# Kernel optimization log

Hardware: AMD Instinct MI355X
Metric: run time of the kernel (lower is better)

The kernel has to match this reference:

```python
import jax, jax.numpy as jnp
import numpy as np

WIDTH = 768
HEAD = 64

def setup_inputs() -> dict:
    key = jax.random.key(0)
    ks = jax.random.split(key, 8)
    x = jax.random.normal(ks[0], (8, 2048, WIDTH), dtype=jnp.float32)
    mask = jax.random.randint(ks[1], (2048, 2048), 0, 2, dtype=jnp.int32)
    s = 1.0 / np.sqrt(WIDTH)
    Wq = jax.random.normal(ks[2], (WIDTH, HEAD), dtype=jnp.float32) * s
    Wk = jax.random.normal(ks[3], (WIDTH, HEAD), dtype=jnp.float32) * s
    Wv = jax.random.normal(ks[4], (WIDTH, HEAD), dtype=jnp.float32) * s
    bq = jax.random.normal(ks[5], (HEAD,), dtype=jnp.float32) * 0.01
    bk = jax.random.normal(ks[6], (HEAD,), dtype=jnp.float32) * 0.01
    bv = jax.random.normal(ks[7], (HEAD,), dtype=jnp.float32) * 0.01
    return {"x": x, "Wq": Wq, "bq": bq, "Wk": Wk, "bk": bk, "Wv": Wv, "bv": bv, "mask": mask}

def reference(x, Wq, bq, Wk, bk, Wv, bv, mask) -> jnp.ndarray:
    # x: [B, N, width]; projections -> [B, N, head]
    Q = jnp.einsum('bnw,wh->bnh', x, Wq) + bq
    K = jnp.einsum('bnw,wh->bnh', x, Wk) + bk
    V = jnp.einsum('bnw,wh->bnh', x, Wv) + bv
    scale = 1.0 / jnp.sqrt(jnp.asarray(Q.shape[-1], dtype=Q.dtype))
    scores = jnp.einsum('bqh,bkh->bqk', Q, K) * scale  # [B, N, N]
    scores = jnp.where(mask == 0, -jnp.inf, scores)
    attn = jax.nn.softmax(scores, axis=-1)
    return jnp.einsum('bqk,bkh->bqh', attn, V)
```

## Files before the change

### kernel.cpp

```cpp
#include <hip/hip_runtime.h>

typedef short  s8v   __attribute__((ext_vector_type(8)));
typedef float  f32x4 __attribute__((ext_vector_type(4)));

#define SEQ 2048
#define WID 768

__device__ __forceinline__ unsigned fbits(float f) {
    union { float f; unsigned u; } v; v.f = f; return v.u;
}
__device__ __forceinline__ float bitsf(unsigned u) {
    union { unsigned u; float f; } v; v.u = u; return v.f;
}
__device__ __forceinline__ unsigned short f2b(float f) {
    unsigned u = fbits(f);
    return (unsigned short)((u + 0x7FFFu + ((u >> 16) & 1u)) >> 16);
}
__device__ __forceinline__ unsigned packRNE(float a, float b) {
    unsigned ta = fbits(a) + 0x7FFFu + ((fbits(a) >> 16) & 1u);
    unsigned tb = fbits(b) + 0x7FFFu + ((fbits(b) >> 16) & 1u);
    return __builtin_amdgcn_perm(tb, ta, 0x07060302u);
}
__device__ __forceinline__ unsigned packTRUNC(float a, float b) {
    return __builtin_amdgcn_perm(fbits(b), fbits(a), 0x07060302u);
}
__device__ __forceinline__ f32x4 zero4() { f32x4 z = {0.f, 0.f, 0.f, 0.f}; return z; }

__device__ __forceinline__ void async16(const unsigned short* g, unsigned short* l) {
    __builtin_amdgcn_global_load_lds(
        (const __attribute__((address_space(1))) unsigned int*)g,
        (__attribute__((address_space(3))) unsigned int*)l, 16, 0, 0);
}

__global__ __launch_bounds__(256) void convert_kernel(
    const float* __restrict__ x, const int* __restrict__ mask,
    const float* __restrict__ Wq, const float* __restrict__ Wk, const float* __restrict__ Wv,
    unsigned short* __restrict__ XF, unsigned short* __restrict__ WF,
    unsigned* __restrict__ PM)
{
    const int tid = threadIdx.x;
    const int blk = blockIdx.x;
    if (blk < 6144) {
        const unsigned s = blk * 256 + tid;
        const unsigned g = s / 1536;
        const unsigned r = s - g * 1536;
        const unsigned kc32 = r >> 6, l = r & 63;
        const unsigned row = g * 16 + (l & 15);
        const unsigned k0 = kc32 * 32 + (l >> 4) * 8;
        float4 f0 = *(const float4*)&x[(size_t)row * WID + k0];
        float4 f1 = *(const float4*)&x[(size_t)row * WID + k0 + 4];
        uint4 w;
        w.x = packRNE(f0.x, f0.y); w.y = packRNE(f0.z, f0.w);
        w.z = packRNE(f1.x, f1.y); w.w = packRNE(f1.z, f1.w);
        *(uint4*)&XF[(size_t)s * 8] = w;
    } else if (blk < 6656) {
        const int b2 = blk - 6144;
        const int gid  = b2 * 4 + (tid >> 6);
        const int lane = tid & 63, quad = lane >> 4, c = lane & 15;
        const int qb = gid >> 5, kb = gid & 31;
        unsigned w = 0;
        #pragma unroll
        for (int mt = 0; mt < 2; ++mt)
            #pragma unroll
            for (int i = 0; i < 4; ++i) {
                const int q = qb * 32 + mt * 16 + quad * 4 + i;
                const int4 mm = *(const int4*)&mask[(size_t)q * SEQ + kb * 64 + 4 * c];
                if (mm.x) w |= 1u << (mt * 16 + i * 4 + 0);
                if (mm.y) w |= 1u << (mt * 16 + i * 4 + 1);
                if (mm.z) w |= 1u << (mt * 16 + i * 4 + 2);
                if (mm.w) w |= 1u << (mt * 16 + i * 4 + 3);
            }
        PM[(size_t)gid * 64 + lane] = w;
    } else {
        const int s2 = (blk - 6656) * 256 + tid;
        const int chunk = s2 >> 6, l = s2 & 63;
        const int ntg = chunk / 24, r = chunk - ntg * 24;
        const int kc = r >> 1, h = r & 1;
        const int mat = ntg >> 2;
        const int col = (ntg & 3) * 16 + (l & 15);
        const int k0 = kc * 64 + h * 32 + (l >> 4) * 8;
        const float* Wm = (mat == 0) ? Wq : (mat == 1) ? Wk : Wv;
        float p[8];
        #pragma unroll
        for (int j = 0; j < 8; ++j) p[j] = Wm[(size_t)(k0 + j) * 64 + col];
        uint4 w;
        w.x = packRNE(p[0], p[1]); w.y = packRNE(p[2], p[3]);
        w.z = packRNE(p[4], p[5]); w.w = packRNE(p[6], p[7]);
        *(uint4*)&WF[(size_t)s2 * 8] = w;
    }
}

__global__ __launch_bounds__(512, 4) void qkv_proj_kernel(
    const unsigned short* __restrict__ XF, const unsigned short* __restrict__ WF,
    const float* __restrict__ bq, const float* __restrict__ bk, const float* __restrict__ bv,
    unsigned short* __restrict__ QF, unsigned short* __restrict__ KF,
    unsigned short* __restrict__ VF)
{
    __shared__ unsigned short AB[2][16384];
    unsigned short (*St)[200] = (unsigned short(*)[200])AB;

    const int tid = threadIdx.x;
    const int wv = tid >> 6, lane = tid & 63, quad = lane >> 4, c = lane & 15;
    const int rg = wv >> 2, cg = wv & 3;
    const int blk = blockIdx.x;
    const int g0 = blk * 4;

    float bias[3];
    #pragma unroll
    for (int nt = 0; nt < 3; ++nt) {
        int col = cg * 48 + nt * 16 + c;
        const float* B = (col < 64) ? bq : (col < 128) ? bk : bv;
        bias[nt] = B[col & 63];
    }

    auto issue = [&](int kc, int b) {
        #pragma unroll
        for (int r = 0; r < 4; ++r) {
            const int d = wv * 4 + r;
            if (d < 8) {
                const int gl = d >> 1, h = d & 1;
                async16(XF + ((size_t)(g0 + gl) * 24 + 2 * kc + h) * 512 + lane * 8,
                        &AB[b][(gl * 2 + h) * 512]);
            } else {
                const int e = d - 8, ntg = e >> 1, h = e & 1;
                async16(WF + (((size_t)ntg * 12 + kc) * 2 + h) * 512 + lane * 8,
                        &AB[b][4096 + (ntg * 2 + h) * 512]);
            }
        }
    };

    f32x4 acc[2][3];
    #pragma unroll
    for (int mt = 0; mt < 2; ++mt)
        #pragma unroll
        for (int nt = 0; nt < 3; ++nt) acc[mt][nt] = zero4();

    issue(0, 0);
    for (int kc = 0; kc < 12; ++kc) {
        const int b = kc & 1;
        __syncthreads();
        if (kc < 11) issue(kc + 1, b ^ 1);

        s8v afr[2][2], bfr[3][2];
        #pragma unroll
        for (int mt = 0; mt < 2; ++mt)
            #pragma unroll
            for (int h = 0; h < 2; ++h)
                afr[mt][h] = *(const s8v*)&AB[b][((rg * 2 + mt) * 2 + h) * 512 + lane * 8];
        #pragma unroll
        for (int nt = 0; nt < 3; ++nt)
            #pragma unroll
            for (int h = 0; h < 2; ++h)
                bfr[nt][h] = *(const s8v*)&AB[b][4096 + ((cg * 3 + nt) * 2 + h) * 512 + lane * 8];
        #pragma unroll
        for (int h = 0; h < 2; ++h)
            #pragma unroll
            for (int mt = 0; mt < 2; ++mt)
                #pragma unroll
                for (int nt = 0; nt < 3; ++nt)
                    acc[mt][nt] = __builtin_amdgcn_mfma_f32_16x16x32_bf16(
                        afr[mt][h], bfr[nt][h], acc[mt][nt], 0, 0, 0);
        __syncthreads();
    }

    #pragma unroll
    for (int mt = 0; mt < 2; ++mt)
        #pragma unroll
        for (int nt = 0; nt < 3; ++nt)
            #pragma unroll
            for (int i = 0; i < 4; ++i)
                St[rg * 32 + mt * 16 + quad * 4 + i][cg * 48 + nt * 16 + c]
                    = f2b(acc[mt][nt][i] + bias[nt]);
    __syncthreads();

    {
        const int g = tid >> 7, ks = (tid >> 6) & 1, l = tid & 63;
        uint4 v = *(uint4*)&St[g * 16 + (l & 15)][ks * 32 + (l >> 4) * 8];
        *(uint4*)&QF[(((size_t)(g0 + g)) * 2 + ks) * 512 + (size_t)l * 8] = v;
    }
    {
        const int ksnt = tid >> 6, l = tid & 63;
        const int ks = ksnt >> 2, nt = ksnt & 3;
        uint4 v = *(uint4*)&St[4 * (l & 15) + nt][64 + ks * 32 + (l >> 4) * 8];
        *(uint4*)&KF[(((size_t)blk * 8 + ksnt) * 64 + l) * 8] = v;
    }
    {
        const int ksnt = tid >> 6, l = tid & 63;
        const int ks = ksnt >> 2, nt = ksnt & 3;
        const int d = 128 + nt * 16 + (l & 15);
        const int r0 = ks * 32 + (l >> 4) * 8;
        unsigned short p[8];
        #pragma unroll
        for (int s = 0; s < 8; ++s) p[s] = St[r0 + s][d];
        uint4 w;
        w.x = (unsigned)p[0] | ((unsigned)p[1] << 16);
        w.y = (unsigned)p[2] | ((unsigned)p[3] << 16);
        w.z = (unsigned)p[4] | ((unsigned)p[5] << 16);
        w.w = (unsigned)p[6] | ((unsigned)p[7] << 16);
        *(uint4*)&VF[(((size_t)blk * 8 + ksnt) * 64 + l) * 8] = w;
    }
}

__global__ __launch_bounds__(1024, 4) void attn_kernel(
    const unsigned short* __restrict__ QF, const unsigned short* __restrict__ KF,
    const unsigned short* __restrict__ VF, const unsigned* __restrict__ PM,
    float* __restrict__ out)
{
    __shared__ unsigned short KV[4][8192];
    __shared__ __align__(16) unsigned char PsOb[36864];
    __shared__ float Lbuf[64];
    unsigned short (*Ps)[16][72] = (unsigned short(*)[16][72])PsOb;
    float (*Obuf)[68]            = (float(*)[68])PsOb;

    const int tid = threadIdx.x;
    const int wv = tid >> 6, lane = tid & 63, quad = lane >> 4, c = lane & 15;
    const int sl = wv & 3, qg = wv >> 2, mt = qg & 1;
    const int blk = blockIdx.x;
    const int bb = blk & 7, qt = blk >> 3;
    const size_t qrow0 = (size_t)bb * SEQ + qt * 64;

    if (tid < 64) Lbuf[tid] = 0.f;

    s8v qf[2];
    {
        const size_t qgrp = (size_t)bb * 128 + qt * 4 + qg;
        #pragma unroll
        for (int ks = 0; ks < 2; ++ks)
            qf[ks] = *(const s8v*)&QF[(qgrp * 2 + ks) * 512 + (size_t)lane * 8];
    }

    f32x4 O[4];
    float lro[4];
    #pragma unroll
    for (int nt = 0; nt < 4; ++nt) O[nt] = zero4();
    #pragma unroll
    for (int i = 0; i < 4; ++i) lro[i] = 0.f;

    auto kv_dma = [&](int kt) {
        const size_t kbg = (size_t)bb * 32 + sl * 8 + kt;
        #pragma unroll
        for (int r = 0; r < 4; ++r) {
            const int d = qg * 4 + r;
            const unsigned short* src = (d < 8)
                ? KF + kbg * 4096 + (d & 7) * 512 + lane * 8
                : VF + kbg * 4096 + (d & 7) * 512 + lane * 8;
            async16(src, &KV[sl][(d >> 3) * 4096 + (d & 7) * 512]);
        }
    };

    kv_dma(0);
    for (int kt = 0; kt < 8; ++kt) {
        const unsigned pm = PM[(size_t)((qt * 2 + (qg >> 1)) * 32 + sl * 8 + kt) * 64 + lane];
        __syncthreads();

        f32x4 S[4];
        #pragma unroll
        for (int nt = 0; nt < 4; ++nt) S[nt] = zero4();
        #pragma unroll
        for (int ks = 0; ks < 2; ++ks) {
            s8v kfr[4];
            #pragma unroll
            for (int nt = 0; nt < 4; ++nt)
                kfr[nt] = *(const s8v*)&KV[sl][((ks * 4 + nt) * 64 + lane) * 8];
            #pragma unroll
            for (int nt = 0; nt < 4; ++nt)
                S[nt] = __builtin_amdgcn_mfma_f32_16x16x32_bf16(qf[ks], kfr[nt], S[nt], 0, 0, 0);
        }

        const unsigned pmh = pm >> (mt * 16);
        #pragma unroll
        for (int i = 0; i < 4; ++i) {
            float p4[4];
            #pragma unroll
            for (int nt = 0; nt < 4; ++nt) {
                float e = exp2f(fmaf(S[nt][i], 0.18033688011112042f, -21.640425613334451f));
                p4[nt] = ((pmh >> (i * 4 + nt)) & 1u) ? e : 0.f;
            }
            unsigned u0 = packTRUNC(p4[0], p4[1]);
            unsigned u1 = packTRUNC(p4[2], p4[3]);
            lro[i] += bitsf(u0 << 16) + bitsf(u0 & 0xFFFF0000u)
                    + bitsf(u1 << 16) + bitsf(u1 & 0xFFFF0000u);
            *(uint2*)&Ps[wv][quad * 4 + i][4 * c] = make_uint2(u0, u1);
        }

        #pragma unroll
        for (int ks = 0; ks < 2; ++ks) {
            s8v a = *(const s8v*)&Ps[wv][c][ks * 32 + quad * 8];
            s8v vfr[4];
            #pragma unroll
            for (int nt = 0; nt < 4; ++nt)
                vfr[nt] = *(const s8v*)&KV[sl][4096 + ((ks * 4 + nt) * 64 + lane) * 8];
            #pragma unroll
            for (int nt = 0; nt < 4; ++nt)
                O[nt] = __builtin_amdgcn_mfma_f32_16x16x32_bf16(a, vfr[nt], O[nt], 0, 0, 0);
        }
        __syncthreads();
        if (kt < 7) kv_dma(kt + 1);
    }

    #pragma unroll
    for (int j = 0; j < 5; ++j) {
        int idx = tid + 1024 * j;
        if (idx < 64 * 68) ((float*)Obuf)[idx] = 0.f;
    }
    __syncthreads();
    #pragma unroll
    for (int i = 0; i < 4; ++i) {
        float l = lro[i];
        l += __shfl_xor(l, 1);
        l += __shfl_xor(l, 2);
        l += __shfl_xor(l, 4);
        l += __shfl_xor(l, 8);
        if (c == 0) atomicAdd(&Lbuf[qg * 16 + quad * 4 + i], l);
        #pragma unroll
        for (int nt = 0; nt < 4; ++nt)
            atomicAdd(&Obuf[qg * 16 + quad * 4 + i][nt * 16 + c], O[nt][i]);
    }
    __syncthreads();
    {
        const int r = tid >> 4, d4 = (tid & 15) * 4;
        const float invL = 1.0f / Lbuf[r];
        float4 v = *(float4*)&Obuf[r][d4];
        float4 o = make_float4(v.x * invL, v.y * invL, v.z * invL, v.w * invL);
        *(float4*)&out[(qrow0 + r) * 64 + d4] = o;
    }
}

extern "C" void kernel_launch(void* const* d_in, const int* in_sizes, int n_in,
                              void* d_out, int out_size, void* d_ws, size_t ws_size,
                              hipStream_t stream)
{
    const float* x    = (const float*)d_in[0];
    const float* Wq   = (const float*)d_in[1];
    const float* bq   = (const float*)d_in[2];
    const float* Wk   = (const float*)d_in[3];
    const float* bk   = (const float*)d_in[4];
    const float* Wv   = (const float*)d_in[5];
    const float* bv   = (const float*)d_in[6];
    const int*   mask = (const int*)d_in[7];
    float* out = (float*)d_out;

    unsigned short* QF = (unsigned short*)d_ws;
    unsigned short* KF = QF + (size_t)16384 * 64;
    unsigned short* VF = KF + (size_t)16384 * 64;
    unsigned short* XF = VF + (size_t)16384 * 64;
    unsigned short* WF = XF + (size_t)16384 * WID;
    unsigned*       PM = (unsigned*)(WF + (size_t)192 * WID);

    convert_kernel<<<6728, 256, 0, stream>>>(x, mask, Wq, Wk, Wv, XF, WF, PM);
    qkv_proj_kernel<<<256, 512, 0, stream>>>(XF, WF, bq, bk, bv, QF, KF, VF);
    attn_kernel<<<256, 1024, 0, stream>>>(QF, KF, VF, PM, out);
}
```

Before: 163.5 us.

## Keep P in registers via transposed QK MFMA and double-buffer K/V tiles

The QK^T MFMA now runs with K as the A operand, so each lane's score fragment already matches the layout the PV MFMA needs for P. This removes the LDS round-trip for the probability tile, and the mask bit-packing and V layout are permuted to match. K/V tiles are double-buffered, with two DMAs issued ahead and explicit vmcnt waits plus raw s_barriers replacing __syncthreads. Mask words and Q are preloaded into registers before the loop. The cost is more LDS for the second K/V buffer, fragile hand-tuned waitcnt logic, and higher register pressure.

```diff
diff --git a/kernel.cpp b/kernel.cpp
--- a/kernel.cpp
+++ b/kernel.cpp
@@ -60,16 +60,17 @@
         const int qb = gid >> 5, kb = gid & 31;
         unsigned w = 0;
         #pragma unroll
-        for (int mt = 0; mt < 2; ++mt)
+        for (int mt = 0; mt < 2; ++mt) {
+            const int q = qb * 32 + mt * 16 + c;
             #pragma unroll
             for (int i = 0; i < 4; ++i) {
-                const int q = qb * 32 + mt * 16 + quad * 4 + i;
-                const int4 mm = *(const int4*)&mask[(size_t)q * SEQ + kb * 64 + 4 * c];
+                const int4 mm = *(const int4*)&mask[(size_t)q * SEQ + kb * 64 + quad * 16 + 4 * i];
                 if (mm.x) w |= 1u << (mt * 16 + i * 4 + 0);
                 if (mm.y) w |= 1u << (mt * 16 + i * 4 + 1);
                 if (mm.z) w |= 1u << (mt * 16 + i * 4 + 2);
                 if (mm.w) w |= 1u << (mt * 16 + i * 4 + 3);
             }
+        }
         PM[(size_t)gid * 64 + lane] = w;
     } else {
         const int s2 = (blk - 6656) * 256 + tid;
@@ -188,7 +189,7 @@
         const int ksnt = tid >> 6, l = tid & 63;
         const int ks = ksnt >> 2, nt = ksnt & 3;
         const int d = 128 + nt * 16 + (l & 15);
-        const int r0 = ks * 32 + (l >> 4) * 8;
+        const int r0 = (l >> 4) * 16 + ks * 8;
         unsigned short p[8];
         #pragma unroll
         for (int s = 0; s < 8; ++s) p[s] = St[r0 + s][d];
@@ -206,11 +207,9 @@
     const unsigned short* __restrict__ VF, const unsigned* __restrict__ PM,
     float* __restrict__ out)
 {
-    __shared__ unsigned short KV[4][8192];
-    __shared__ __align__(16) unsigned char PsOb[36864];
+    __shared__ unsigned short KV[4][2][8192];
+    __shared__ float Obuf[64][68];
     __shared__ float Lbuf[64];
-    unsigned short (*Ps)[16][72] = (unsigned short(*)[16][72])PsOb;
-    float (*Obuf)[68]            = (float(*)[68])PsOb;
 
     const int tid = threadIdx.x;
     const int wv = tid >> 6, lane = tid & 63, quad = lane >> 4, c = lane & 15;
@@ -221,22 +220,33 @@
 
     if (tid < 64) Lbuf[tid] = 0.f;
 
-    s8v qf[2];
+    unsigned pm[8];
+    #pragma unroll
+    for (int kt = 0; kt < 8; ++kt)
+        pm[kt] = PM[(size_t)(((qt * 2 + (qg >> 1)) * 32 + sl * 8 + kt) * 64 + lane)];
+
+    union Q8 { s8v v; unsigned w[4]; } qf[2];
     {
         const size_t qgrp = (size_t)bb * 128 + qt * 4 + qg;
         #pragma unroll
         for (int ks = 0; ks < 2; ++ks)
-            qf[ks] = *(const s8v*)&QF[(qgrp * 2 + ks) * 512 + (size_t)lane * 8];
-    }
+            qf[ks].v = *(const s8v*)&QF[(qgrp * 2 + ks) * 512 + (size_t)lane * 8];
+    }
+    asm volatile("s_waitcnt vmcnt(0)" ::: "memory");
+    #pragma unroll
+    for (int kt = 0; kt < 8; ++kt) asm volatile("" : "+v"(pm[kt]));
+    #pragma unroll
+    for (int ks = 0; ks < 2; ++ks)
+        #pragma unroll
+        for (int j = 0; j < 4; ++j) asm volatile("" : "+v"(qf[ks].w[j]));
+    __builtin_amdgcn_sched_barrier(0);
 
     f32x4 O[4];
-    float lro[4];
+    float lro = 0.f;
     #pragma unroll
     for (int nt = 0; nt < 4; ++nt) O[nt] = zero4();
-    #pragma unroll
-    for (int i = 0; i < 4; ++i) lro[i] = 0.f;
-
-    auto kv_dma = [&](int kt) {
+
+    auto kv_dma = [&](int kt, int b) {
         const size_t kbg = (size_t)bb * 32 + sl * 8 + kt;
         #pragma unroll
         for (int r = 0; r < 4; ++r) {
@@ -244,14 +254,20 @@
             const unsigned short* src = (d < 8)
                 ? KF + kbg * 4096 + (d & 7) * 512 + lane * 8
                 : VF + kbg * 4096 + (d & 7) * 512 + lane * 8;
-            async16(src, &KV[sl][(d >> 3) * 4096 + (d & 7) * 512]);
+            async16(src, &KV[sl][b][(d >> 3) * 4096 + (d & 7) * 512]);
         }
     };
 
-    kv_dma(0);
+    kv_dma(0, 0);
+    kv_dma(1, 1);
+
+    #pragma unroll
     for (int kt = 0; kt < 8; ++kt) {
-        const unsigned pm = PM[(size_t)((qt * 2 + (qg >> 1)) * 32 + sl * 8 + kt) * 64 + lane];
-        __syncthreads();
+        const int b = kt & 1;
+        if (kt < 7) asm volatile("s_waitcnt vmcnt(4)" ::: "memory");
+        else        asm volatile("s_waitcnt vmcnt(0)" ::: "memory");
+        __builtin_amdgcn_sched_barrier(0);
+        __builtin_amdgcn_s_barrier();
 
         f32x4 S[4];
         #pragma unroll
@@ -261,41 +277,44 @@
             s8v kfr[4];
             #pragma unroll
             for (int nt = 0; nt < 4; ++nt)
-                kfr[nt] = *(const s8v*)&KV[sl][((ks * 4 + nt) * 64 + lane) * 8];
+                kfr[nt] = *(const s8v*)&KV[sl][b][((ks * 4 + nt) * 64 + lane) * 8];
             #pragma unroll
             for (int nt = 0; nt < 4; ++nt)
-                S[nt] = __builtin_amdgcn_mfma_f32_16x16x32_bf16(qf[ks], kfr[nt], S[nt], 0, 0, 0);
-        }
-
-        const unsigned pmh = pm >> (mt * 16);
-        #pragma unroll
-        for (int i = 0; i < 4; ++i) {
-            float p4[4];
+                S[nt] = __builtin_amdgcn_mfma_f32_16x16x32_bf16(kfr[nt], qf[ks].v, S[nt], 0, 0, 0);
+        }
+
+        const unsigned pmh = pm[kt] >> (mt * 16);
+        float p[4][4];
+        #pragma unroll
+        for (int i = 0; i < 4; ++i)
             #pragma unroll
             for (int nt = 0; nt < 4; ++nt) {
                 float e = exp2f(fmaf(S[nt][i], 0.18033688011112042f, -21.640425613334451f));
-                p4[nt] = ((pmh >> (i * 4 + nt)) & 1u) ? e : 0.f;
+                p[nt][i] = ((pmh >> (i * 4 + nt)) & 1u) ? e : 0.f;
             }
-            unsigned u0 = packTRUNC(p4[0], p4[1]);
-            unsigned u1 = packTRUNC(p4[2], p4[3]);
-            lro[i] += bitsf(u0 << 16) + bitsf(u0 & 0xFFFF0000u)
-                    + bitsf(u1 << 16) + bitsf(u1 & 0xFFFF0000u);
-            *(uint2*)&Ps[wv][quad * 4 + i][4 * c] = make_uint2(u0, u1);
+        union { unsigned w[8]; s8v v[2]; } P;
+        #pragma unroll
+        for (int j = 0; j < 8; ++j) {
+            unsigned uu = packTRUNC(p[2 * (j & 1)][j >> 1], p[2 * (j & 1) + 1][j >> 1]);
+            P.w[j] = uu;
+            lro += bitsf(uu << 16) + bitsf(uu & 0xFFFF0000u);
         }
 
         #pragma unroll
         for (int ks = 0; ks < 2; ++ks) {
-            s8v a = *(const s8v*)&Ps[wv][c][ks * 32 + quad * 8];
             s8v vfr[4];
             #pragma unroll
             for (int nt = 0; nt < 4; ++nt)
-                vfr[nt] = *(const s8v*)&KV[sl][4096 + ((ks * 4 + nt) * 64 + lane) * 8];
+                vfr[nt] = *(const s8v*)&KV[sl][b][4096 + ((ks * 4 + nt) * 64 + lane) * 8];
             #pragma unroll
             for (int nt = 0; nt < 4; ++nt)
-                O[nt] = __builtin_amdgcn_mfma_f32_16x16x32_bf16(a, vfr[nt], O[nt], 0, 0, 0);
-        }
-        __syncthreads();
-        if (kt < 7) kv_dma(kt + 1);
+                O[nt] = __builtin_amdgcn_mfma_f32_16x16x32_bf16(P.v[ks], vfr[nt], O[nt], 0, 0, 0);
+        }
+
+        if (kt < 6) {
+            __builtin_amdgcn_s_barrier();
+            kv_dma(kt + 2, b);
+        }
     }
 
     #pragma unroll
@@ -304,18 +323,18 @@
         if (idx < 64 * 68) ((float*)Obuf)[idx] = 0.f;
     }
     __syncthreads();
-    #pragma unroll
-    for (int i = 0; i < 4; ++i) {
-        float l = lro[i];
-        l += __shfl_xor(l, 1);
-        l += __shfl_xor(l, 2);
-        l += __shfl_xor(l, 4);
-        l += __shfl_xor(l, 8);
-        if (c == 0) atomicAdd(&Lbuf[qg * 16 + quad * 4 + i], l);
+
+    {
+        float l = lro;
+        l += __shfl_xor(l, 16);
+        l += __shfl_xor(l, 32);
+        if (quad == 0) atomicAdd(&Lbuf[qg * 16 + c], l);
+    }
+    #pragma unroll
+    for (int i = 0; i < 4; ++i)
         #pragma unroll
         for (int nt = 0; nt < 4; ++nt)
             atomicAdd(&Obuf[qg * 16 + quad * 4 + i][nt * 16 + c], O[nt][i]);
-    }
     __syncthreads();
     {
         const int r = tid >> 4, d4 = (tid & 15) * 4;
```

After: 162.6 us. Within noise of the previous version (-0.6%).
